# Kernel tuning notes

Measured on AMD Instinct MI355X. Metric: run time of the kernel, lower is better.

## Reference

```python
import jax, jax.numpy as jnp
import numpy as np


def setup_inputs() -> dict:
    key = jax.random.key(0)
    k = jax.random.split(key, 5)
    bs, n_heads, ch, n_obj, emb = 4, 8, 64, 8, 64
    ih = iw = 32
    T = ih * iw
    return {
        "qkv": jax.random.normal(k[0], (bs, 3 * n_heads * ch, T), dtype=jnp.float32),
        "bboxes": jax.random.uniform(k[1], (bs, n_obj, 5), dtype=jnp.float32),
        "null_prompt_emb": jax.random.normal(k[2], (bs, emb, T), dtype=jnp.float32),
        "prompt_emb": jax.random.normal(k[3], (bs, emb, T), dtype=jnp.float32),
        "W_prompt": jax.random.normal(k[4], (3 * n_heads * ch, emb), dtype=jnp.float32) * 0.02,
        "n_heads": n_heads,
        "image_h": ih,
        "image_w": iw,
    }


def _region_masks(bboxes, h, w):
    # Faithful translation of get_region: bbox unpacked as (x, y, width, height, obj_idx).
    # Returns float masks [b, n_obj, h*w].
    x, y, bw, bh = bboxes[..., 0], bboxes[..., 1], bboxes[..., 2], bboxes[..., 3]
    i0 = jnp.minimum(float(h) - 1.0, jnp.floor(y * h))
    j0 = jnp.minimum(float(w) - 1.0, jnp.floor(x * w))
    i1 = i0 + jnp.maximum(1.0, jnp.ceil(bh * h))
    j1 = j0 + jnp.maximum(1.0, jnp.ceil(bw * w))
    ii = jnp.arange(h, dtype=jnp.float32)
    jj = jnp.arange(w, dtype=jnp.float32)
    mi = (ii >= i0[..., None]) & (ii < i1[..., None])          # [b, n, h]
    mj = (jj >= j0[..., None]) & (jj < j1[..., None])          # [b, n, w]
    m = (mi[..., :, None] & mj[..., None, :]).astype(jnp.float32)  # [b, n, h, w]
    return m.reshape(m.shape[0], m.shape[1], h * w)


def reference(qkv, bboxes, null_prompt_emb, prompt_emb, W_prompt, n_heads, image_h, image_w):
    bs, width, T = qkv.shape
    ch = width // (3 * n_heads)
    scale = float(ch) ** -0.25  # 1/sqrt(sqrt(ch))

    def split3(x):
        x = x.reshape(bs * n_heads, 3 * ch, T)
        return x[:, :ch], x[:, ch:2 * ch], x[:, 2 * ch:]

    q, k, v = split3(qkv)
    # to_prompt_token is a 1x1 Conv1d (no bias) == matmul over the channel dim
    nq, nk, nv = split3(jnp.einsum('oc,bct->bot', W_prompt, null_prompt_emb))
    pq, pk, pv = split3(jnp.einsum('oc,bct->bot', W_prompt, prompt_emb))

    def attn(qh, kh, vh, col_mask=None):
        w = jnp.einsum('bct,bcs->bts', qh * scale, kh * scale)
        if col_mask is not None:
            w = jnp.where(col_mask[:, None, :] > 0.5, w, -1e9)
        w = jax.nn.softmax(w.astype(jnp.float32), axis=-1).astype(qh.dtype)
        return jnp.einsum('bts,bcs->btc', w, vh)  # [bs*heads, T, ch]

    # global (null-prompt) attention
    a_null = attn(q + nq, k + nk, v + nv)

    # per-object masked attention, blended by region masks
    masks = _region_masks(bboxes, image_h, image_w)       # [bs, n_obj, T]
    masks = jnp.repeat(masks, n_heads, axis=0)            # [(bs*heads), n_obj, T]
    qf, kf, vf = q + pq, k + pk, v + pv
    a_fg = jnp.zeros_like(a_null)
    counter = jnp.zeros((bs * n_heads, T, 1), dtype=jnp.float32)
    for o in range(masks.shape[1]):  # small fixed loop over objects
        m = masks[:, o]                                   # [bs*heads, T]
        a_fg = a_fg + m[:, :, None] * attn(qf, kf, vf, col_mask=m)
        counter = counter + m[:, :, None]
    fg = counter > 0.5
    a_final = jnp.where(fg, a_fg, a_null) / jnp.where(fg, counter, 1.0)
    return jnp.transpose(a_final, (0, 2, 1)).reshape(bs, n_heads * ch, T)
```

## Files before the change

### kernel.cpp

```cpp
#include <hip/hip_runtime.h>
#include <math.h>

#define BS 4
#define NH 8
#define TT 1024
#define WROWS 1536
#define NOBJ 8
#define NT 65536

#define QNT_OFF  0
#define KNT_OFF  2097152
#define VNCS_OFF 4194304
#define QFT_OFF  6291456
#define KFT_OFF  8388608
#define VFT_OFF  10485760

typedef __attribute__((ext_vector_type(8))) short short8;
typedef __attribute__((ext_vector_type(4))) float v4f;

__device__ __forceinline__ short f2bf(float f) {
    unsigned u = __float_as_uint(f);
    u = (u + 0x7FFF + ((u >> 16) & 1)) >> 16;
    return (short)u;
}
__device__ __forceinline__ unsigned p2(float a, float b) {
    return (unsigned)(unsigned short)f2bf(a) | ((unsigned)(unsigned short)f2bf(b) << 16);
}

__device__ __forceinline__ void get_region(const float* __restrict__ bb,
                                           int& i0, int& j0, int& hh, int& ww) {
    float x = bb[0], y = bb[1], bw = bb[2], bh = bb[3];
    float i0f = fminf(31.0f, floorf(y * 32.0f));
    float j0f = fminf(31.0f, floorf(x * 32.0f));
    float i1f = i0f + fmaxf(1.0f, ceilf(bh * 32.0f));
    float j1f = j0f + fmaxf(1.0f, ceilf(bw * 32.0f));
    i0 = (int)i0f; j0 = (int)j0f;
    int i1 = min(32, (int)i1f);
    int j1 = min(32, (int)j1f);
    hh = i1 - i0; ww = j1 - j0;
}

__global__ __launch_bounds__(256)
void fuse_kernel(const float* __restrict__ qkv, const float* __restrict__ nEmb,
                 const float* __restrict__ pEmb, const float* __restrict__ W,
                 short* __restrict__ wsS) {
    __shared__ float WtT[64][68];
    __shared__ float En[64][64];
    __shared__ float Ep[64][64];
    short* sbuf = (short*)&WtT[0][0];
    int t0 = blockIdx.x * 64;
    int r0 = blockIdx.y * 64;
    int b  = blockIdx.z;
    int tid = threadIdx.x;
    int half = tid >> 4;
    int q4 = (tid & 15) * 4;
#pragma unroll
    for (int p = 0; p < 4; ++p) {
        int rr = p * 16 + half;
        float4 w4 = *(const float4*)&W[(r0 + rr) * 64 + q4];
        WtT[q4 + 0][rr] = w4.x; WtT[q4 + 1][rr] = w4.y;
        WtT[q4 + 2][rr] = w4.z; WtT[q4 + 3][rr] = w4.w;
        int e = p * 16 + half;
        *(float4*)&En[e][q4] = *(const float4*)&nEmb[(b * 64 + e) * TT + t0 + q4];
        *(float4*)&Ep[e][q4] = *(const float4*)&pEmb[(b * 64 + e) * TT + t0 + q4];
    }
    __syncthreads();
    int tr = tid >> 4, tc = tid & 15;
    float an[4][4] = {{0.f}}, ap[4][4] = {{0.f}};
#pragma unroll 8
    for (int e = 0; e < 64; ++e) {
        float4 w4 = *(const float4*)&WtT[e][tr * 4];
        float4 n4 = *(const float4*)&En[e][tc * 4];
        float4 p4 = *(const float4*)&Ep[e][tc * 4];
        float w[4]  = {w4.x, w4.y, w4.z, w4.w};
        float nn[4] = {n4.x, n4.y, n4.z, n4.w};
        float pp[4] = {p4.x, p4.y, p4.z, p4.w};
#pragma unroll
        for (int i = 0; i < 4; ++i)
#pragma unroll
            for (int j = 0; j < 4; ++j) {
                an[i][j] += w[i] * nn[j];
                ap[i][j] += w[i] * pp[j];
            }
    }
    int sec = (r0 % 192) / 64;
    int h = r0 / 192, bh = b * 8 + h;
    float sc = (sec == 0) ? 0.125f : 1.0f;
#pragma unroll
    for (int i = 0; i < 4; ++i) {
        int r = r0 + tr * 4 + i;
        float4 x4 = *(const float4*)&qkv[(b * WROWS + r) * TT + t0 + tc * 4];
        an[i][0] = (an[i][0] + x4.x) * sc; an[i][1] = (an[i][1] + x4.y) * sc;
        an[i][2] = (an[i][2] + x4.z) * sc; an[i][3] = (an[i][3] + x4.w) * sc;
        ap[i][0] = (ap[i][0] + x4.x) * sc; ap[i][1] = (ap[i][1] + x4.y) * sc;
        ap[i][2] = (ap[i][2] + x4.z) * sc; ap[i][3] = (ap[i][3] + x4.w) * sc;
    }
    if (sec == 2) {
        short* Vn = wsS + VNCS_OFF + bh * NT;
#pragma unroll
        for (int i = 0; i < 4; ++i) {
            int c = tr * 4 + i;
            uint2 pk; pk.x = p2(an[i][0], an[i][1]); pk.y = p2(an[i][2], an[i][3]);
            *(uint2*)&Vn[c * TT + t0 + tc * 4] = pk;
        }
        short* dst = wsS + VFT_OFF + bh * NT + t0 * 64;
        __syncthreads();
#pragma unroll
        for (int i = 0; i < 4; ++i)
#pragma unroll
            for (int j = 0; j < 4; ++j)
                sbuf[(tc * 4 + j) * 72 + tr * 4 + i] = f2bf(ap[i][j]);
        __syncthreads();
#pragma unroll
        for (int rep = 0; rep < 2; ++rep) {
            int idx = rep * 256 + tid; int tl = idx >> 3, c8 = idx & 7;
            *(short8*)&dst[tl * 64 + c8 * 8] = *(const short8*)&sbuf[tl * 72 + c8 * 8];
        }
    } else {
        short* dn = wsS + (sec == 0 ? QNT_OFF : KNT_OFF) + bh * NT + t0 * 64;
        short* df = wsS + (sec == 0 ? QFT_OFF : KFT_OFF) + bh * NT + t0 * 64;
        __syncthreads();
#pragma unroll
        for (int i = 0; i < 4; ++i)
#pragma unroll
            for (int j = 0; j < 4; ++j)
                sbuf[(tc * 4 + j) * 72 + tr * 4 + i] = f2bf(an[i][j]);
        __syncthreads();
#pragma unroll
        for (int rep = 0; rep < 2; ++rep) {
            int idx = rep * 256 + tid; int tl = idx >> 3, c8 = idx & 7;
            *(short8*)&dn[tl * 64 + c8 * 8] = *(const short8*)&sbuf[tl * 72 + c8 * 8];
        }
        __syncthreads();
#pragma unroll
        for (int i = 0; i < 4; ++i)
#pragma unroll
            for (int j = 0; j < 4; ++j)
                sbuf[(tc * 4 + j) * 72 + tr * 4 + i] = f2bf(ap[i][j]);
        __syncthreads();
#pragma unroll
        for (int rep = 0; rep < 2; ++rep) {
            int idx = rep * 256 + tid; int tl = idx >> 3, c8 = idx & 7;
            *(short8*)&df[tl * 64 + c8 * 8] = *(const short8*)&sbuf[tl * 72 + c8 * 8];
        }
    }
}

__global__ __launch_bounds__(256)
void attn_fused(const short* __restrict__ wsS, const float* __restrict__ bboxes,
                float* __restrict__ out) {
    __shared__ __align__(16) short lds[13824];
    __shared__ unsigned short tmap[1024];
    short* Qs = lds;
    short* Ks = lds + 4608;
    short* Vs = lds + 9216;
    int rt = blockIdx.x, bh = blockIdx.y;
    int b = bh >> 3, h = bh & 7;
    int t0 = rt * 64;
    int tid = threadIdx.x;
    int w = tid >> 6, lane = tid & 63, ln = lane & 15, qd = lane >> 4;
    const short* QnT = wsS + QNT_OFF + bh * NT;
    const short* KnT = wsS + KNT_OFF + bh * NT;
    const short* Vn  = wsS + VNCS_OFF + bh * NT;
    const short* QfT = wsS + QFT_OFF + bh * NT;
    const short* KfT = wsS + KFT_OFF + bh * NT;
    const short* VfT = wsS + VFT_OFF + bh * NT;
    int sidx = tid, scell = sidx >> 3, sc8 = sidx & 7;
    int sidx2 = 256 + tid, scell2 = sidx2 >> 3, sc82 = sidx2 & 7;

    *(short8*)&Qs[scell * 72 + sc8 * 8]  = *(const short8*)&QnT[(t0 + scell) * 64 + sc8 * 8];
    *(short8*)&Qs[scell2 * 72 + sc82 * 8] = *(const short8*)&QnT[(t0 + scell2) * 64 + sc82 * 8];
    __syncthreads();
    short8 aq0 = *(const short8*)&Qs[(16 * w + ln) * 72 + qd * 8];
    short8 aq1 = *(const short8*)&Qs[(16 * w + ln) * 72 + 32 + qd * 8];
    v4f O[4]; float l[4];
#pragma unroll
    for (int r = 0; r < 4; ++r) l[r] = 0.f;
#pragma unroll
    for (int cc = 0; cc < 4; ++cc) O[cc] = (v4f){0.f, 0.f, 0.f, 0.f};
    short8 kreg[2], vreg[2];
    kreg[0] = *(const short8*)&KnT[scell * 64 + sc8 * 8];
    kreg[1] = *(const short8*)&KnT[scell2 * 64 + sc82 * 8];
    vreg[0] = *(const short8*)&Vn[scell * TT + sc8 * 8];
    vreg[1] = *(const short8*)&Vn[scell2 * TT + sc82 * 8];
    for (int ct = 0; ct < 16; ++ct) {
        __syncthreads();
        *(short8*)&Ks[scell * 72 + sc8 * 8]  = kreg[0];
        *(short8*)&Ks[scell2 * 72 + sc82 * 8] = kreg[1];
        *(short8*)&Vs[scell * 72 + sc8 * 8]  = vreg[0];
        *(short8*)&Vs[scell2 * 72 + sc82 * 8] = vreg[1];
        __syncthreads();
        if (ct < 15) {
            int s0 = (ct + 1) * 64;
            kreg[0] = *(const short8*)&KnT[(s0 + scell) * 64 + sc8 * 8];
            kreg[1] = *(const short8*)&KnT[(s0 + scell2) * 64 + sc82 * 8];
            vreg[0] = *(const short8*)&Vn[scell * TT + s0 + sc8 * 8];
            vreg[1] = *(const short8*)&Vn[scell2 * TT + s0 + sc82 * 8];
        }
        v4f S[4];
#pragma unroll
        for (int nn = 0; nn < 4; ++nn) {
            short8 b0 = *(const short8*)&Ks[(nn * 16 + ln) * 72 + qd * 8];
            short8 b1 = *(const short8*)&Ks[(nn * 16 + ln) * 72 + 32 + qd * 8];
            v4f z = (v4f){0.f, 0.f, 0.f, 0.f};
            z = __builtin_amdgcn_mfma_f32_16x16x32_bf16(aq0, b0, z, 0, 0, 0);
            z = __builtin_amdgcn_mfma_f32_16x16x32_bf16(aq1, b1, z, 0, 0, 0);
            S[nn] = z;
        }
#pragma unroll
        for (int r = 0; r < 4; ++r) {
            float e0 = __expf(S[0][r]);
            float e1 = __expf(S[1][r]);
            float e2 = __expf(S[2][r]);
            float e3 = __expf(S[3][r]);
            l[r] += e0 + e1 + e2 + e3;
            int prow = (w * 16 + 4 * qd + r) * 72;
            Qs[prow +  0 + ln] = f2bf(e0);
            Qs[prow + 16 + ln] = f2bf(e1);
            Qs[prow + 32 + ln] = f2bf(e2);
            Qs[prow + 48 + ln] = f2bf(e3);
        }
        short8 ap0 = *(const short8*)&Qs[(w * 16 + ln) * 72 + qd * 8];
        short8 ap1 = *(const short8*)&Qs[(w * 16 + ln) * 72 + 32 + qd * 8];
#pragma unroll
        for (int cc = 0; cc < 4; ++cc) {
            short8 bv0 = *(const short8*)&Vs[(cc * 16 + ln) * 72 + qd * 8];
            short8 bv1 = *(const short8*)&Vs[(cc * 16 + ln) * 72 + 32 + qd * 8];
            O[cc] = __builtin_amdgcn_mfma_f32_16x16x32_bf16(ap0, bv0, O[cc], 0, 0, 0);
            O[cc] = __builtin_amdgcn_mfma_f32_16x16x32_bf16(ap1, bv1, O[cc], 0, 0, 0);
        }
    }
    v4f Onull[4];
#pragma unroll
    for (int r = 0; r < 4; ++r) {
        float rs = l[r];
        rs += __shfl_xor(rs, 1, 64);
        rs += __shfl_xor(rs, 2, 64);
        rs += __shfl_xor(rs, 4, 64);
        rs += __shfl_xor(rs, 8, 64);
        float inv = 1.0f / rs;
#pragma unroll
        for (int cc = 0; cc < 4; ++cc) Onull[cc][r] = O[cc][r] * inv;
    }

    __syncthreads();
    *(short8*)&Qs[scell * 72 + sc8 * 8]  = *(const short8*)&QfT[(t0 + scell) * 64 + sc8 * 8];
    *(short8*)&Qs[scell2 * 72 + sc82 * 8] = *(const short8*)&QfT[(t0 + scell2) * 64 + sc82 * 8];
    __syncthreads();
    aq0 = *(const short8*)&Qs[(16 * w + ln) * 72 + qd * 8];
    aq1 = *(const short8*)&Qs[(16 * w + ln) * 72 + 32 + qd * 8];
    v4f Oacc[4]; float cnt[4];
#pragma unroll
    for (int r = 0; r < 4; ++r) cnt[r] = 0.f;
#pragma unroll
    for (int cc = 0; cc < 4; ++cc) Oacc[cc] = (v4f){0.f, 0.f, 0.f, 0.f};

    for (int o = 0; o < NOBJ; ++o) {
        int i0, j0, hh, ww;
        get_region(&bboxes[(b * NOBJ + o) * 5], i0, j0, hh, ww);
        int i1 = i0 + hh;
        if (i0 > 2 * rt + 1 || i1 <= 2 * rt) continue;
        int R = hh * ww;
        for (int idx = tid; idx < R; idx += 256) {
            int ri = idx / ww; int rj = idx - ri * ww;
            tmap[idx] = (unsigned short)((i0 + ri) * 32 + j0 + rj);
        }
        __syncthreads();
#pragma unroll
        for (int r = 0; r < 4; ++r) l[r] = 0.f;
#pragma unroll
        for (int cc = 0; cc < 4; ++cc) O[cc] = (v4f){0.f, 0.f, 0.f, 0.f};
        int nct = (R + 63) >> 6;
        {
            int tA = tmap[min(scell, R - 1)];
            int tB = tmap[min(scell2, R - 1)];
            kreg[0] = *(const short8*)&KfT[tA * 64 + sc8 * 8];
            kreg[1] = *(const short8*)&KfT[tB * 64 + sc82 * 8];
            vreg[0] = *(const short8*)&VfT[tA * 64 + sc8 * 8];
            vreg[1] = *(const short8*)&VfT[tB * 64 + sc82 * 8];
        }
        for (int ct = 0; ct < nct; ++ct) {
            int sb = ct * 64;
            __syncthreads();
            *(short8*)&Ks[scell * 72 + sc8 * 8]  = kreg[0];
            *(short8*)&Ks[scell2 * 72 + sc82 * 8] = kreg[1];
#pragma unroll
            for (int jj = 0; jj < 8; ++jj) {
                int j = (jj + sc8) & 7;
                Vs[(sc8 * 8 + j) * 72 + scell] = vreg[0][j];
            }
#pragma unroll
            for (int jj = 0; jj < 8; ++jj) {
                int j = (jj + sc82) & 7;
                Vs[(sc82 * 8 + j) * 72 + scell2] = vreg[1][j];
            }
            __syncthreads();
            if (ct + 1 < nct) {
                int s0 = sb + 64;
                int tA = tmap[min(s0 + scell, R - 1)];
                int tB = tmap[min(s0 + scell2, R - 1)];
                kreg[0] = *(const short8*)&KfT[tA * 64 + sc8 * 8];
                kreg[1] = *(const short8*)&KfT[tB * 64 + sc82 * 8];
                vreg[0] = *(const short8*)&VfT[tA * 64 + sc8 * 8];
                vreg[1] = *(const short8*)&VfT[tB * 64 + sc82 * 8];
            }
            v4f S[4];
#pragma unroll
            for (int nn = 0; nn < 4; ++nn) {
                short8 b0 = *(const short8*)&Ks[(nn * 16 + ln) * 72 + qd * 8];
                short8 b1 = *(const short8*)&Ks[(nn * 16 + ln) * 72 + 32 + qd * 8];
                v4f z = (v4f){0.f, 0.f, 0.f, 0.f};
                z = __builtin_amdgcn_mfma_f32_16x16x32_bf16(aq0, b0, z, 0, 0, 0);
                z = __builtin_amdgcn_mfma_f32_16x16x32_bf16(aq1, b1, z, 0, 0, 0);
                S[nn] = z;
            }
            float v0 = (sb +  0 + ln) < R ? 1.f : 0.f;
            float v1 = (sb + 16 + ln) < R ? 1.f : 0.f;
            float v2 = (sb + 32 + ln) < R ? 1.f : 0.f;
            float v3 = (sb + 48 + ln) < R ? 1.f : 0.f;
#pragma unroll
            for (int r = 0; r < 4; ++r) {
                float e0 = __expf(S[0][r]) * v0;
                float e1 = __expf(S[1][r]) * v1;
                float e2 = __expf(S[2][r]) * v2;
                float e3 = __expf(S[3][r]) * v3;
                l[r] += e0 + e1 + e2 + e3;
                int prow = (w * 16 + 4 * qd + r) * 72;
                Qs[prow +  0 + ln] = f2bf(e0);
                Qs[prow + 16 + ln] = f2bf(e1);
                Qs[prow + 32 + ln] = f2bf(e2);
                Qs[prow + 48 + ln] = f2bf(e3);
            }
            short8 ap0 = *(const short8*)&Qs[(w * 16 + ln) * 72 + qd * 8];
            short8 ap1 = *(const short8*)&Qs[(w * 16 + ln) * 72 + 32 + qd * 8];
#pragma unroll
            for (int cc = 0; cc < 4; ++cc) {
                short8 bv0 = *(const short8*)&Vs[(cc * 16 + ln) * 72 + qd * 8];
                short8 bv1 = *(const short8*)&Vs[(cc * 16 + ln) * 72 + 32 + qd * 8];
                O[cc] = __builtin_amdgcn_mfma_f32_16x16x32_bf16(ap0, bv0, O[cc], 0, 0, 0);
                O[cc] = __builtin_amdgcn_mfma_f32_16x16x32_bf16(ap1, bv1, O[cc], 0, 0, 0);
            }
        }
#pragma unroll
        for (int r = 0; r < 4; ++r) {
            float rs = l[r];
            rs += __shfl_xor(rs, 1, 64);
            rs += __shfl_xor(rs, 2, 64);
            rs += __shfl_xor(rs, 4, 64);
            rs += __shfl_xor(rs, 8, 64);
            float inv = 1.0f / rs;
            int t = t0 + 16 * w + 4 * qd + r;
            int ti = t >> 5, tj = t & 31;
            bool in = (ti >= i0) && (ti < i1) && (tj >= j0) && (tj < j0 + ww);
            if (in) {
                cnt[r] += 1.f;
#pragma unroll
                for (int cc = 0; cc < 4; ++cc) Oacc[cc][r] += O[cc][r] * inv;
            }
        }
    }

    __syncthreads();
    float* Ot = (float*)lds;
#pragma unroll
    for (int r = 0; r < 4; ++r) {
        int tl = 16 * w + 4 * qd + r;
        float icnt = cnt[r] > 0.f ? 1.0f / cnt[r] : 0.f;
#pragma unroll
        for (int cc = 0; cc < 4; ++cc) {
            float val = cnt[r] > 0.f ? Oacc[cc][r] * icnt : Onull[cc][r];
            Ot[(cc * 16 + ln) * 68 + tl] = val;
        }
    }
    __syncthreads();
    int obase = (b * 512 + h * 64) * TT + t0;
#pragma unroll
    for (int rep = 0; rep < 4; ++rep) {
        int idx = rep * 256 + tid; int c = idx >> 4, t4 = (idx & 15) * 4;
        *(float4*)&out[obase + c * TT + t4] = *(float4*)&Ot[c * 68 + t4];
    }
}

extern "C" void kernel_launch(void* const* d_in, const int* in_sizes, int n_in,
                              void* d_out, int out_size, void* d_ws, size_t ws_size,
                              hipStream_t stream) {
    const float* qkv    = (const float*)d_in[0];
    const float* bboxes = (const float*)d_in[1];
    const float* nEmb   = (const float*)d_in[2];
    const float* pEmb   = (const float*)d_in[3];
    const float* W      = (const float*)d_in[4];
    short* wsS = (short*)d_ws;
    float* out = (float*)d_out;

    fuse_kernel<<<dim3(16, 24, 4), 256, 0, stream>>>(qkv, nEmb, pEmb, W, wsS);
    attn_fused<<<dim3(16, 32), 256, 0, stream>>>(wsS, bboxes, out);
}
```

Before: 161.9 us.

## Split key dimension across two wave groups in attention kernel (512 threads)

The attention kernel now runs 512 threads per block. Two groups of four waves each process alternate 64-key tiles for the same 64 query rows, and their partial outputs and row sums are combined through LDS at the end. The goal is more waves per block to hide latency and raise occupancy, since the grid is only 512 blocks. In exchange there are extra LDS reductions and barriers per object, and LDS use per block doubles.

```diff
diff --git a/kernel.cpp b/kernel.cpp
--- a/kernel.cpp
+++ b/kernel.cpp
@@ -38,6 +38,14 @@
     int i1 = min(32, (int)i1f);
     int j1 = min(32, (int)j1f);
     hh = i1 - i0; ww = j1 - j0;
+}
+
+__device__ __forceinline__ float rowsum16(float x) {
+    x += __shfl_xor(x, 1, 64);
+    x += __shfl_xor(x, 2, 64);
+    x += __shfl_xor(x, 4, 64);
+    x += __shfl_xor(x, 8, 64);
+    return x;
 }
 
 __global__ __launch_bounds__(256)
@@ -146,33 +154,39 @@
     }
 }
 
-__global__ __launch_bounds__(256)
+__global__ __launch_bounds__(512, 4)
 void attn_fused(const short* __restrict__ wsS, const float* __restrict__ bboxes,
                 float* __restrict__ out) {
-    __shared__ __align__(16) short lds[13824];
+    __shared__ __align__(16) short lds[27648];
     __shared__ unsigned short tmap[1024];
-    short* Qs = lds;
-    short* Ks = lds + 4608;
-    short* Vs = lds + 9216;
+    __shared__ float lbuf[64];
+    short* Ps = lds;
+    short* Ks = lds + 9216;
+    short* Vs = lds + 18432;
+    float* fO1 = (float*)(lds + 18432);
+    float* Ot  = (float*)lds;
+
     int rt = blockIdx.x, bh = blockIdx.y;
     int b = bh >> 3, h = bh & 7;
     int t0 = rt * 64;
     int tid = threadIdx.x;
     int w = tid >> 6, lane = tid & 63, ln = lane & 15, qd = lane >> 4;
+    int rw = w & 3;
+    int wg = w >> 2;
     const short* QnT = wsS + QNT_OFF + bh * NT;
     const short* KnT = wsS + KNT_OFF + bh * NT;
     const short* Vn  = wsS + VNCS_OFF + bh * NT;
     const short* QfT = wsS + QFT_OFF + bh * NT;
     const short* KfT = wsS + KFT_OFF + bh * NT;
     const short* VfT = wsS + VFT_OFF + bh * NT;
-    int sidx = tid, scell = sidx >> 3, sc8 = sidx & 7;
-    int sidx2 = 256 + tid, scell2 = sidx2 >> 3, sc82 = sidx2 & 7;
-
-    *(short8*)&Qs[scell * 72 + sc8 * 8]  = *(const short8*)&QnT[(t0 + scell) * 64 + sc8 * 8];
-    *(short8*)&Qs[scell2 * 72 + sc82 * 8] = *(const short8*)&QnT[(t0 + scell2) * 64 + sc82 * 8];
-    __syncthreads();
-    short8 aq0 = *(const short8*)&Qs[(16 * w + ln) * 72 + qd * 8];
-    short8 aq1 = *(const short8*)&Qs[(16 * w + ln) * 72 + 32 + qd * 8];
+    int scell = tid >> 3, sc8 = tid & 7;
+    short* Kb = Ks + wg * 4608;
+    short* Vb = Vs + wg * 4608;
+
+    *(short8*)&Ps[scell * 72 + sc8 * 8] = *(const short8*)&QnT[(t0 + scell) * 64 + sc8 * 8];
+    __syncthreads();
+    short8 aq0 = *(const short8*)&Ps[(16 * rw + ln) * 72 + qd * 8];
+    short8 aq1 = *(const short8*)&Ps[(16 * rw + ln) * 72 + 32 + qd * 8];
     v4f O[4]; float l[4];
 #pragma unroll
     for (int r = 0; r < 4; ++r) l[r] = 0.f;
@@ -180,28 +194,28 @@
     for (int cc = 0; cc < 4; ++cc) O[cc] = (v4f){0.f, 0.f, 0.f, 0.f};
     short8 kreg[2], vreg[2];
     kreg[0] = *(const short8*)&KnT[scell * 64 + sc8 * 8];
-    kreg[1] = *(const short8*)&KnT[scell2 * 64 + sc82 * 8];
+    kreg[1] = *(const short8*)&KnT[(64 + scell) * 64 + sc8 * 8];
     vreg[0] = *(const short8*)&Vn[scell * TT + sc8 * 8];
-    vreg[1] = *(const short8*)&Vn[scell2 * TT + sc82 * 8];
-    for (int ct = 0; ct < 16; ++ct) {
-        __syncthreads();
-        *(short8*)&Ks[scell * 72 + sc8 * 8]  = kreg[0];
-        *(short8*)&Ks[scell2 * 72 + sc82 * 8] = kreg[1];
-        *(short8*)&Vs[scell * 72 + sc8 * 8]  = vreg[0];
-        *(short8*)&Vs[scell2 * 72 + sc82 * 8] = vreg[1];
-        __syncthreads();
-        if (ct < 15) {
-            int s0 = (ct + 1) * 64;
+    vreg[1] = *(const short8*)&Vn[scell * TT + 64 + sc8 * 8];
+    for (int it = 0; it < 8; ++it) {
+        __syncthreads();
+        *(short8*)&Ks[scell * 72 + sc8 * 8]        = kreg[0];
+        *(short8*)&Ks[4608 + scell * 72 + sc8 * 8] = kreg[1];
+        *(short8*)&Vs[scell * 72 + sc8 * 8]        = vreg[0];
+        *(short8*)&Vs[4608 + scell * 72 + sc8 * 8] = vreg[1];
+        __syncthreads();
+        if (it < 7) {
+            int s0 = (it + 1) * 128;
             kreg[0] = *(const short8*)&KnT[(s0 + scell) * 64 + sc8 * 8];
-            kreg[1] = *(const short8*)&KnT[(s0 + scell2) * 64 + sc82 * 8];
+            kreg[1] = *(const short8*)&KnT[(s0 + 64 + scell) * 64 + sc8 * 8];
             vreg[0] = *(const short8*)&Vn[scell * TT + s0 + sc8 * 8];
-            vreg[1] = *(const short8*)&Vn[scell2 * TT + s0 + sc82 * 8];
+            vreg[1] = *(const short8*)&Vn[scell * TT + s0 + 64 + sc8 * 8];
         }
         v4f S[4];
 #pragma unroll
         for (int nn = 0; nn < 4; ++nn) {
-            short8 b0 = *(const short8*)&Ks[(nn * 16 + ln) * 72 + qd * 8];
-            short8 b1 = *(const short8*)&Ks[(nn * 16 + ln) * 72 + 32 + qd * 8];
+            short8 b0 = *(const short8*)&Kb[(nn * 16 + ln) * 72 + qd * 8];
+            short8 b1 = *(const short8*)&Kb[(nn * 16 + ln) * 72 + 32 + qd * 8];
             v4f z = (v4f){0.f, 0.f, 0.f, 0.f};
             z = __builtin_amdgcn_mfma_f32_16x16x32_bf16(aq0, b0, z, 0, 0, 0);
             z = __builtin_amdgcn_mfma_f32_16x16x32_bf16(aq1, b1, z, 0, 0, 0);
@@ -215,40 +229,32 @@
             float e3 = __expf(S[3][r]);
             l[r] += e0 + e1 + e2 + e3;
             int prow = (w * 16 + 4 * qd + r) * 72;
-            Qs[prow +  0 + ln] = f2bf(e0);
-            Qs[prow + 16 + ln] = f2bf(e1);
-            Qs[prow + 32 + ln] = f2bf(e2);
-            Qs[prow + 48 + ln] = f2bf(e3);
-        }
-        short8 ap0 = *(const short8*)&Qs[(w * 16 + ln) * 72 + qd * 8];
-        short8 ap1 = *(const short8*)&Qs[(w * 16 + ln) * 72 + 32 + qd * 8];
+            Ps[prow +  0 + ln] = f2bf(e0);
+            Ps[prow + 16 + ln] = f2bf(e1);
+            Ps[prow + 32 + ln] = f2bf(e2);
+            Ps[prow + 48 + ln] = f2bf(e3);
+        }
+        short8 ap0 = *(const short8*)&Ps[(w * 16 + ln) * 72 + qd * 8];
+        short8 ap1 = *(const short8*)&Ps[(w * 16 + ln) * 72 + 32 + qd * 8];
 #pragma unroll
         for (int cc = 0; cc < 4; ++cc) {
-            short8 bv0 = *(const short8*)&Vs[(cc * 16 + ln) * 72 + qd * 8];
-            short8 bv1 = *(const short8*)&Vs[(cc * 16 + ln) * 72 + 32 + qd * 8];
+            short8 bv0 = *(const short8*)&Vb[(cc * 16 + ln) * 72 + qd * 8];
+            short8 bv1 = *(const short8*)&Vb[(cc * 16 + ln) * 72 + 32 + qd * 8];
             O[cc] = __builtin_amdgcn_mfma_f32_16x16x32_bf16(ap0, bv0, O[cc], 0, 0, 0);
             O[cc] = __builtin_amdgcn_mfma_f32_16x16x32_bf16(ap1, bv1, O[cc], 0, 0, 0);
         }
     }
-    v4f Onull[4];
-#pragma unroll
-    for (int r = 0; r < 4; ++r) {
-        float rs = l[r];
-        rs += __shfl_xor(rs, 1, 64);
-        rs += __shfl_xor(rs, 2, 64);
-        rs += __shfl_xor(rs, 4, 64);
-        rs += __shfl_xor(rs, 8, 64);
-        float inv = 1.0f / rs;
-#pragma unroll
-        for (int cc = 0; cc < 4; ++cc) Onull[cc][r] = O[cc][r] * inv;
-    }
-
-    __syncthreads();
-    *(short8*)&Qs[scell * 72 + sc8 * 8]  = *(const short8*)&QfT[(t0 + scell) * 64 + sc8 * 8];
-    *(short8*)&Qs[scell2 * 72 + sc82 * 8] = *(const short8*)&QfT[(t0 + scell2) * 64 + sc82 * 8];
-    __syncthreads();
-    aq0 = *(const short8*)&Qs[(16 * w + ln) * 72 + qd * 8];
-    aq1 = *(const short8*)&Qs[(16 * w + ln) * 72 + 32 + qd * 8];
+    v4f Onull[4]; float lnull[4];
+#pragma unroll
+    for (int r = 0; r < 4; ++r) lnull[r] = rowsum16(l[r]);
+#pragma unroll
+    for (int cc = 0; cc < 4; ++cc) Onull[cc] = O[cc];
+
+    __syncthreads();
+    *(short8*)&Ps[scell * 72 + sc8 * 8] = *(const short8*)&QfT[(t0 + scell) * 64 + sc8 * 8];
+    __syncthreads();
+    aq0 = *(const short8*)&Ps[(16 * rw + ln) * 72 + qd * 8];
+    aq1 = *(const short8*)&Ps[(16 * rw + ln) * 72 + 32 + qd * 8];
     v4f Oacc[4]; float cnt[4];
 #pragma unroll
     for (int r = 0; r < 4; ++r) cnt[r] = 0.f;
@@ -261,7 +267,7 @@
         int i1 = i0 + hh;
         if (i0 > 2 * rt + 1 || i1 <= 2 * rt) continue;
         int R = hh * ww;
-        for (int idx = tid; idx < R; idx += 256) {
+        for (int idx = tid; idx < R; idx += 512) {
             int ri = idx / ww; int rj = idx - ri * ww;
             tmap[idx] = (unsigned short)((i0 + ri) * 32 + j0 + rj);
         }
@@ -271,19 +277,20 @@
 #pragma unroll
         for (int cc = 0; cc < 4; ++cc) O[cc] = (v4f){0.f, 0.f, 0.f, 0.f};
         int nct = (R + 63) >> 6;
+        int npair = (nct + 1) >> 1;
         {
             int tA = tmap[min(scell, R - 1)];
-            int tB = tmap[min(scell2, R - 1)];
+            int tB = tmap[min(64 + scell, R - 1)];
             kreg[0] = *(const short8*)&KfT[tA * 64 + sc8 * 8];
-            kreg[1] = *(const short8*)&KfT[tB * 64 + sc82 * 8];
+            kreg[1] = *(const short8*)&KfT[tB * 64 + sc8 * 8];
             vreg[0] = *(const short8*)&VfT[tA * 64 + sc8 * 8];
-            vreg[1] = *(const short8*)&VfT[tB * 64 + sc82 * 8];
-        }
-        for (int ct = 0; ct < nct; ++ct) {
-            int sb = ct * 64;
+            vreg[1] = *(const short8*)&VfT[tB * 64 + sc8 * 8];
+        }
+        for (int p = 0; p < npair; ++p) {
+            int sbw = (2 * p + wg) * 64;
             __syncthreads();
-            *(short8*)&Ks[scell * 72 + sc8 * 8]  = kreg[0];
-            *(short8*)&Ks[scell2 * 72 + sc82 * 8] = kreg[1];
+            *(short8*)&Ks[scell * 72 + sc8 * 8]        = kreg[0];
+            *(short8*)&Ks[4608 + scell * 72 + sc8 * 8] = kreg[1];
 #pragma unroll
             for (int jj = 0; jj < 8; ++jj) {
                 int j = (jj + sc8) & 7;
@@ -291,33 +298,33 @@
             }
 #pragma unroll
             for (int jj = 0; jj < 8; ++jj) {
-                int j = (jj + sc82) & 7;
-                Vs[(sc82 * 8 + j) * 72 + scell2] = vreg[1][j];
+                int j = (jj + sc8) & 7;
+                Vs[4608 + (sc8 * 8 + j) * 72 + scell] = vreg[1][j];
             }
             __syncthreads();
-            if (ct + 1 < nct) {
-                int s0 = sb + 64;
+            if (p + 1 < npair) {
+                int s0 = (2 * p + 2) * 64;
                 int tA = tmap[min(s0 + scell, R - 1)];
-                int tB = tmap[min(s0 + scell2, R - 1)];
+                int tB = tmap[min(s0 + 64 + scell, R - 1)];
                 kreg[0] = *(const short8*)&KfT[tA * 64 + sc8 * 8];
-                kreg[1] = *(const short8*)&KfT[tB * 64 + sc82 * 8];
+                kreg[1] = *(const short8*)&KfT[tB * 64 + sc8 * 8];
                 vreg[0] = *(const short8*)&VfT[tA * 64 + sc8 * 8];
-                vreg[1] = *(const short8*)&VfT[tB * 64 + sc82 * 8];
+                vreg[1] = *(const short8*)&VfT[tB * 64 + sc8 * 8];
             }
             v4f S[4];
 #pragma unroll
             for (int nn = 0; nn < 4; ++nn) {
-                short8 b0 = *(const short8*)&Ks[(nn * 16 + ln) * 72 + qd * 8];
-                short8 b1 = *(const short8*)&Ks[(nn * 16 + ln) * 72 + 32 + qd * 8];
+                short8 b0 = *(const short8*)&Kb[(nn * 16 + ln) * 72 + qd * 8];
+                short8 b1 = *(const short8*)&Kb[(nn * 16 + ln) * 72 + 32 + qd * 8];
                 v4f z = (v4f){0.f, 0.f, 0.f, 0.f};
                 z = __builtin_amdgcn_mfma_f32_16x16x32_bf16(aq0, b0, z, 0, 0, 0);
                 z = __builtin_amdgcn_mfma_f32_16x16x32_bf16(aq1, b1, z, 0, 0, 0);
                 S[nn] = z;
             }
-            float v0 = (sb +  0 + ln) < R ? 1.f : 0.f;
-            float v1 = (sb + 16 + ln) < R ? 1.f : 0.f;
-            float v2 = (sb + 32 + ln) < R ? 1.f : 0.f;
-            float v3 = (sb + 48 + ln) < R ? 1.f : 0.f;
+            float v0 = (sbw +  0 + ln) < R ? 1.f : 0.f;
+            float v1 = (sbw + 16 + ln) < R ? 1.f : 0.f;
+            float v2 = (sbw + 32 + ln) < R ? 1.f : 0.f;
+            float v3 = (sbw + 48 + ln) < R ? 1.f : 0.f;
 #pragma unroll
             for (int r = 0; r < 4; ++r) {
                 float e0 = __expf(S[0][r]) * v0;
@@ -326,57 +333,86 @@
                 float e3 = __expf(S[3][r]) * v3;
                 l[r] += e0 + e1 + e2 + e3;
                 int prow = (w * 16 + 4 * qd + r) * 72;
-                Qs[prow +  0 + ln] = f2bf(e0);
-                Qs[prow + 16 + ln] = f2bf(e1);
-                Qs[prow + 32 + ln] = f2bf(e2);
-                Qs[prow + 48 + ln] = f2bf(e3);
-            }
-            short8 ap0 = *(const short8*)&Qs[(w * 16 + ln) * 72 + qd * 8];
-            short8 ap1 = *(const short8*)&Qs[(w * 16 + ln) * 72 + 32 + qd * 8];
+                Ps[prow +  0 + ln] = f2bf(e0);
+                Ps[prow + 16 + ln] = f2bf(e1);
+                Ps[prow + 32 + ln] = f2bf(e2);
+                Ps[prow + 48 + ln] = f2bf(e3);
+            }
+            short8 ap0 = *(const short8*)&Ps[(w * 16 + ln) * 72 + qd * 8];
+            short8 ap1 = *(const short8*)&Ps[(w * 16 + ln) * 72 + 32 + qd * 8];
 #pragma unroll
             for (int cc = 0; cc < 4; ++cc) {
-                short8 bv0 = *(const short8*)&Vs[(cc * 16 + ln) * 72 + qd * 8];
-                short8 bv1 = *(const short8*)&Vs[(cc * 16 + ln) * 72 + 32 + qd * 8];
+                short8 bv0 = *(const short8*)&Vb[(cc * 16 + ln) * 72 + qd * 8];
+                short8 bv1 = *(const short8*)&Vb[(cc * 16 + ln) * 72 + 32 + qd * 8];
                 O[cc] = __builtin_amdgcn_mfma_f32_16x16x32_bf16(ap0, bv0, O[cc], 0, 0, 0);
                 O[cc] = __builtin_amdgcn_mfma_f32_16x16x32_bf16(ap1, bv1, O[cc], 0, 0, 0);
             }
         }
+        __syncthreads();
+        if (wg == 1) {
+#pragma unroll
+            for (int r = 0; r < 4; ++r) {
+                float rs = rowsum16(l[r]);
+                int row = 16 * rw + 4 * qd + r;
+                if (ln == 0) lbuf[row] = rs;
+#pragma unroll
+                for (int cc = 0; cc < 4; ++cc)
+                    fO1[row * 68 + cc * 16 + ln] = O[cc][r];
+            }
+        }
+        __syncthreads();
+        if (wg == 0) {
+#pragma unroll
+            for (int r = 0; r < 4; ++r) {
+                int row = 16 * rw + 4 * qd + r;
+                float rs = rowsum16(l[r]) + lbuf[row];
+                float inv = 1.0f / rs;
+                int t = t0 + row;
+                int ti = t >> 5, tj = t & 31;
+                bool in = (ti >= i0) && (ti < i1) && (tj >= j0) && (tj < j0 + ww);
+                if (in) {
+                    cnt[r] += 1.f;
+#pragma unroll
+                    for (int cc = 0; cc < 4; ++cc)
+                        Oacc[cc][r] += (O[cc][r] + fO1[row * 68 + cc * 16 + ln]) * inv;
+                }
+            }
+        }
+    }
+
+    __syncthreads();
+    if (wg == 1) {
 #pragma unroll
         for (int r = 0; r < 4; ++r) {
-            float rs = l[r];
-            rs += __shfl_xor(rs, 1, 64);
-            rs += __shfl_xor(rs, 2, 64);
-            rs += __shfl_xor(rs, 4, 64);
-            rs += __shfl_xor(rs, 8, 64);
-            float inv = 1.0f / rs;
-            int t = t0 + 16 * w + 4 * qd + r;
-            int ti = t >> 5, tj = t & 31;
-            bool in = (ti >= i0) && (ti < i1) && (tj >= j0) && (tj < j0 + ww);
-            if (in) {
-                cnt[r] += 1.f;
-#pragma unroll
-                for (int cc = 0; cc < 4; ++cc) Oacc[cc][r] += O[cc][r] * inv;
-            }
-        }
-    }
-
-    __syncthreads();
-    float* Ot = (float*)lds;
-#pragma unroll
-    for (int r = 0; r < 4; ++r) {
-        int tl = 16 * w + 4 * qd + r;
-        float icnt = cnt[r] > 0.f ? 1.0f / cnt[r] : 0.f;
-#pragma unroll
-        for (int cc = 0; cc < 4; ++cc) {
-            float val = cnt[r] > 0.f ? Oacc[cc][r] * icnt : Onull[cc][r];
-            Ot[(cc * 16 + ln) * 68 + tl] = val;
+            int row = 16 * rw + 4 * qd + r;
+            if (ln == 0) lbuf[row] = lnull[r];
+#pragma unroll
+            for (int cc = 0; cc < 4; ++cc)
+                fO1[row * 68 + cc * 16 + ln] = Onull[cc][r];
+        }
+    }
+    __syncthreads();
+    if (wg == 0) {
+#pragma unroll
+        for (int r = 0; r < 4; ++r) {
+            int row = 16 * rw + 4 * qd + r;
+            float lt = lnull[r] + lbuf[row];
+            float invn = 1.0f / lt;
+            bool fg = cnt[r] > 0.f;
+            float icnt = fg ? 1.0f / cnt[r] : 0.f;
+#pragma unroll
+            for (int cc = 0; cc < 4; ++cc) {
+                float vnull = (Onull[cc][r] + fO1[row * 68 + cc * 16 + ln]) * invn;
+                float val = fg ? Oacc[cc][r] * icnt : vnull;
+                Ot[(cc * 16 + ln) * 68 + row] = val;
+            }
         }
     }
     __syncthreads();
     int obase = (b * 512 + h * 64) * TT + t0;
 #pragma unroll
-    for (int rep = 0; rep < 4; ++rep) {
-        int idx = rep * 256 + tid; int c = idx >> 4, t4 = (idx & 15) * 4;
+    for (int rep = 0; rep < 2; ++rep) {
+        int idx = rep * 512 + tid; int c = idx >> 4, t4 = (idx & 15) * 4;
         *(float4*)&out[obase + c * TT + t4] = *(float4*)&Ot[c * 68 + t4];
     }
 }
@@ -393,5 +429,5 @@
     float* out = (float*)d_out;
 
     fuse_kernel<<<dim3(16, 24, 4), 256, 0, stream>>>(qkv, nEmb, pEmb, W, wsS);
-    attn_fused<<<dim3(16, 32), 256, 0, stream>>>(wsS, bboxes, out);
-}
+    attn_fused<<<dim3(16, 32), 512, 0, stream>>>(wsS, bboxes, out);
+}
```

Result: slower. 205.3 us (+26.8%).

## Use native exp2 with folded log2e scale, packed bf16 converts, permuted key layout

Applied to the files above, without the earlier changes.

Folds log2(e) into the Q scale so the softmax can use the raw v_exp_f32 (exp2) instruction instead of __expf. It replaces the manual bf16 rounding with the hardware v_cvt_pk_bf16_f32 instruction and writes P as packed 64-bit stores. To allow those packed stores, the key axis is permuted, applied consistently to the stored V (null V in the pre-pass, fg V in LDS). This cuts ALU and LDS-store work in the softmax inner loop, but the permutation must match exactly across the producer kernel and the attention kernel.

```diff
diff --git a/kernel.cpp b/kernel.cpp
--- a/kernel.cpp
+++ b/kernel.cpp
@@ -1,5 +1,4 @@
 #include <hip/hip_runtime.h>
-#include <math.h>
 
 #define BS 4
 #define NH 8
@@ -23,9 +22,17 @@
     u = (u + 0x7FFF + ((u >> 16) & 1)) >> 16;
     return (short)u;
 }
-__device__ __forceinline__ unsigned p2(float a, float b) {
-    return (unsigned)(unsigned short)f2bf(a) | ((unsigned)(unsigned short)f2bf(b) << 16);
-}
+__device__ __forceinline__ unsigned cvtpk(float a, float b) {
+    unsigned u;
+    asm("v_cvt_pk_bf16_f32 %0, %1, %2" : "=v"(u) : "v"(a), "v"(b));
+    return u;
+}
+__device__ __forceinline__ float fexp2(float x) {
+    float r;
+    asm("v_exp_f32 %0, %1" : "=v"(r) : "v"(x));
+    return r;
+}
+__device__ __forceinline__ int pi64(int s) { return 4 * (s & 15) + (s >> 4); }
 
 __device__ __forceinline__ void get_region(const float* __restrict__ bb,
                                            int& i0, int& j0, int& hh, int& ww) {
@@ -85,7 +92,7 @@
     }
     int sec = (r0 % 192) / 64;
     int h = r0 / 192, bh = b * 8 + h;
-    float sc = (sec == 0) ? 0.125f : 1.0f;
+    float sc = (sec == 0) ? 0.18033688f : 1.0f;
 #pragma unroll
     for (int i = 0; i < 4; ++i) {
         int r = r0 + tr * 4 + i;
@@ -97,19 +104,27 @@
     }
     if (sec == 2) {
         short* Vn = wsS + VNCS_OFF + bh * NT;
-#pragma unroll
-        for (int i = 0; i < 4; ++i) {
-            int c = tr * 4 + i;
-            uint2 pk; pk.x = p2(an[i][0], an[i][1]); pk.y = p2(an[i][2], an[i][3]);
-            *(uint2*)&Vn[c * TT + t0 + tc * 4] = pk;
+        __syncthreads();
+#pragma unroll
+        for (int i = 0; i < 4; ++i)
+#pragma unroll
+            for (int j = 0; j < 4; ++j) {
+                int p = tc * 4 + j;
+                sbuf[(tr * 4 + i) * 72 + pi64(p)] = f2bf(an[i][j]);
+            }
+        __syncthreads();
+#pragma unroll
+        for (int rep = 0; rep < 2; ++rep) {
+            int idx = rep * 256 + tid; int cl = idx >> 3, c8 = idx & 7;
+            *(short8*)&Vn[cl * TT + t0 + c8 * 8] = *(const short8*)&sbuf[cl * 72 + c8 * 8];
         }
         short* dst = wsS + VFT_OFF + bh * NT + t0 * 64;
         __syncthreads();
 #pragma unroll
-        for (int i = 0; i < 4; ++i)
-#pragma unroll
-            for (int j = 0; j < 4; ++j)
-                sbuf[(tc * 4 + j) * 72 + tr * 4 + i] = f2bf(ap[i][j]);
+        for (int j = 0; j < 4; ++j) {
+            uint2 u; u.x = cvtpk(ap[0][j], ap[1][j]); u.y = cvtpk(ap[2][j], ap[3][j]);
+            *(uint2*)&sbuf[(tc * 4 + j) * 72 + tr * 4] = u;
+        }
         __syncthreads();
 #pragma unroll
         for (int rep = 0; rep < 2; ++rep) {
@@ -121,10 +136,10 @@
         short* df = wsS + (sec == 0 ? QFT_OFF : KFT_OFF) + bh * NT + t0 * 64;
         __syncthreads();
 #pragma unroll
-        for (int i = 0; i < 4; ++i)
-#pragma unroll
-            for (int j = 0; j < 4; ++j)
-                sbuf[(tc * 4 + j) * 72 + tr * 4 + i] = f2bf(an[i][j]);
+        for (int j = 0; j < 4; ++j) {
+            uint2 u; u.x = cvtpk(an[0][j], an[1][j]); u.y = cvtpk(an[2][j], an[3][j]);
+            *(uint2*)&sbuf[(tc * 4 + j) * 72 + tr * 4] = u;
+        }
         __syncthreads();
 #pragma unroll
         for (int rep = 0; rep < 2; ++rep) {
@@ -133,10 +148,10 @@
         }
         __syncthreads();
 #pragma unroll
-        for (int i = 0; i < 4; ++i)
-#pragma unroll
-            for (int j = 0; j < 4; ++j)
-                sbuf[(tc * 4 + j) * 72 + tr * 4 + i] = f2bf(ap[i][j]);
+        for (int j = 0; j < 4; ++j) {
+            uint2 u; u.x = cvtpk(ap[0][j], ap[1][j]); u.y = cvtpk(ap[2][j], ap[3][j]);
+            *(uint2*)&sbuf[(tc * 4 + j) * 72 + tr * 4] = u;
+        }
         __syncthreads();
 #pragma unroll
         for (int rep = 0; rep < 2; ++rep) {
@@ -209,16 +224,13 @@
         }
 #pragma unroll
         for (int r = 0; r < 4; ++r) {
-            float e0 = __expf(S[0][r]);
-            float e1 = __expf(S[1][r]);
-            float e2 = __expf(S[2][r]);
-            float e3 = __expf(S[3][r]);
-            l[r] += e0 + e1 + e2 + e3;
-            int prow = (w * 16 + 4 * qd + r) * 72;
-            Qs[prow +  0 + ln] = f2bf(e0);
-            Qs[prow + 16 + ln] = f2bf(e1);
-            Qs[prow + 32 + ln] = f2bf(e2);
-            Qs[prow + 48 + ln] = f2bf(e3);
+            float e0 = fexp2(S[0][r]);
+            float e1 = fexp2(S[1][r]);
+            float e2 = fexp2(S[2][r]);
+            float e3 = fexp2(S[3][r]);
+            l[r] += (e0 + e1) + (e2 + e3);
+            uint2 u; u.x = cvtpk(e0, e1); u.y = cvtpk(e2, e3);
+            *(uint2*)&Qs[(w * 16 + 4 * qd + r) * 72 + 4 * ln] = u;
         }
         short8 ap0 = *(const short8*)&Qs[(w * 16 + ln) * 72 + qd * 8];
         short8 ap1 = *(const short8*)&Qs[(w * 16 + ln) * 72 + 32 + qd * 8];
@@ -279,6 +291,7 @@
             vreg[0] = *(const short8*)&VfT[tA * 64 + sc8 * 8];
             vreg[1] = *(const short8*)&VfT[tB * 64 + sc82 * 8];
         }
+        int pA = pi64(scell), pB = pi64(scell2);
         for (int ct = 0; ct < nct; ++ct) {
             int sb = ct * 64;
             __syncthreads();
@@ -287,12 +300,12 @@
 #pragma unroll
             for (int jj = 0; jj < 8; ++jj) {
                 int j = (jj + sc8) & 7;
-                Vs[(sc8 * 8 + j) * 72 + scell] = vreg[0][j];
+                Vs[(sc8 * 8 + j) * 72 + pA] = vreg[0][j];
             }
 #pragma unroll
             for (int jj = 0; jj < 8; ++jj) {
                 int j = (jj + sc82) & 7;
-                Vs[(sc82 * 8 + j) * 72 + scell2] = vreg[1][j];
+                Vs[(sc82 * 8 + j) * 72 + pB] = vreg[1][j];
             }
             __syncthreads();
             if (ct + 1 < nct) {
@@ -320,16 +333,13 @@
             float v3 = (sb + 48 + ln) < R ? 1.f : 0.f;
 #pragma unroll
             for (int r = 0; r < 4; ++r) {
-                float e0 = __expf(S[0][r]) * v0;
-                float e1 = __expf(S[1][r]) * v1;
-                float e2 = __expf(S[2][r]) * v2;
-                float e3 = __expf(S[3][r]) * v3;
-                l[r] += e0 + e1 + e2 + e3;
-                int prow = (w * 16 + 4 * qd + r) * 72;
-                Qs[prow +  0 + ln] = f2bf(e0);
-                Qs[prow + 16 + ln] = f2bf(e1);
-                Qs[prow + 32 + ln] = f2bf(e2);
-                Qs[prow + 48 + ln] = f2bf(e3);
+                float e0 = fexp2(S[0][r]) * v0;
+                float e1 = fexp2(S[1][r]) * v1;
+                float e2 = fexp2(S[2][r]) * v2;
+                float e3 = fexp2(S[3][r]) * v3;
+                l[r] += (e0 + e1) + (e2 + e3);
+                uint2 u; u.x = cvtpk(e0, e1); u.y = cvtpk(e2, e3);
+                *(uint2*)&Qs[(w * 16 + 4 * qd + r) * 72 + 4 * ln] = u;
             }
             short8 ap0 = *(const short8*)&Qs[(w * 16 + ln) * 72 + qd * 8];
             short8 ap1 = *(const short8*)&Qs[(w * 16 + ln) * 72 + 32 + qd * 8];
```

Result: faster. 154.4 us (-4.7%).
